# Kernel optimization log

Hardware: AMD Instinct MI355X
Metric: run time of the kernel (lower is better)

Reference implementation:

```python
import jax, jax.numpy as jnp
import numpy as np

N = 16384

def setup_inputs() -> dict:
    key = jax.random.key(0)
    k1, k2, k3 = jax.random.split(key, 3)
    risk_scores = jax.random.normal(k1, (N,), dtype=jnp.float32)
    survival_times = jax.random.normal(k2, (N,), dtype=jnp.float32)
    # 0/1 event indicator (1 = event observed, 0 = censored)
    events = (jax.random.uniform(k3, (N,)) < 0.5).astype(jnp.float32)
    return {"risk_scores": risk_scores, "survival_times": survival_times, "events": events}

def reference(risk_scores, survival_times, events):
    # Risk-set matrix: R[i, j] = 1 if T[j] >= T[i] (vectorized version of the
    # original O(n^2) double Python loop).
    R = (survival_times[None, :] >= survival_times[:, None]).astype(risk_scores.dtype)  # [n, n]
    exp_theta = jnp.exp(risk_scores)                # [n]
    # sum_j exp(theta_j) * R[i, j]  ->  matvec
    risk_set_sum = R @ exp_theta                    # [n]
    loss = -jnp.mean((risk_scores - jnp.log(risk_set_sum)) * events)
    return loss
```

## Files before the change

### kernel.cpp

```cpp
#include <hip/hip_runtime.h>
#include <math.h>

#define NF 16384
#define NB 4096
#define NBLK 64
#define TPB 256
#define CHUNK (NB/TPB)
#define NZ (4 + 3*NB)
#define BLOCK 256

__device__ __forceinline__ int bucket_of(float t) {
    int b = (int)((t + 6.0f) * (NB / 12.0f));
    return min(max(b, 0), NB - 1);
}

__global__ void surv_zero(int* __restrict__ w) {
    int i = blockIdx.x * TPB + threadIdx.x;
    if (i < NZ) w[i] = 0;
}

__global__ __launch_bounds__(TPB) void surv_pipe(
        const float* __restrict__ theta, const float* __restrict__ T,
        const float* __restrict__ events,
        int* __restrict__ bar, int* __restrict__ ticket, float* __restrict__ accum,
        int* __restrict__ hcnt, float* __restrict__ hE, int* __restrict__ rel,
        float2* __restrict__ sorted, float* __restrict__ out) {
    __shared__ int   pfx[NB + 1];
    __shared__ float sfx[NB];
    __shared__ int   sc[TPB];
    __shared__ float se[TPB];

    const int tid = threadIdx.x;
    const int i   = blockIdx.x * TPB + tid;

    const float Ti = T[i];
    const float Ei = expf(theta[i]);
    const int   bi = bucket_of(Ti);
    atomicAdd(&hcnt[bi], 1);
    atomicAdd(&hE[bi], Ei);

    __syncthreads();
    if (tid == 0) {
        __hip_atomic_fetch_add(&bar[0], 1, __ATOMIC_RELEASE, __HIP_MEMORY_SCOPE_AGENT);
        while (__hip_atomic_load(&bar[0], __ATOMIC_ACQUIRE, __HIP_MEMORY_SCOPE_AGENT) < NBLK)
            __builtin_amdgcn_s_sleep(8);
    }
    __syncthreads();

    int lc[CHUNK]; float le[CHUNK];
    const int base = tid * CHUNK;
    int cs = 0; float es = 0.f;
    #pragma unroll
    for (int k = 0; k < CHUNK; ++k) {
        lc[k] = hcnt[base + k];
        le[k] = hE[base + k];
        cs += lc[k]; es += le[k];
    }
    sc[tid] = cs; se[tid] = es;
    __syncthreads();
    for (int s = 1; s < TPB; s <<= 1) {
        int   a = (tid >= s)      ? sc[tid - s] : 0;
        float f = (tid + s < TPB) ? se[tid + s] : 0.f;
        __syncthreads();
        sc[tid] += a; se[tid] += f;
        __syncthreads();
    }
    {   int run = sc[tid] - cs;
        #pragma unroll
        for (int k = 0; k < CHUNK; ++k) { pfx[base + k] = run; run += lc[k]; }
        if (tid == TPB - 1) pfx[NB] = run;
    }
    {   float rs = se[tid] - es;
        #pragma unroll
        for (int k = CHUNK - 1; k >= 0; --k) { sfx[base + k] = rs; rs += le[k]; }
    }
    __syncthreads();

    const int pos = pfx[bi] + atomicAdd(&rel[bi], 1);
    sorted[pos] = make_float2(Ti, Ei);

    __syncthreads();
    if (tid == 0) {
        __hip_atomic_fetch_add(&bar[1], 1, __ATOMIC_RELEASE, __HIP_MEMORY_SCOPE_AGENT);
        while (__hip_atomic_load(&bar[1], __ATOMIC_ACQUIRE, __HIP_MEMORY_SCOPE_AGENT) < NBLK)
            __builtin_amdgcn_s_sleep(8);
    }
    __syncthreads();

    float risk = sfx[bi];
    const int p1 = pfx[bi + 1];
    for (int p = pfx[bi]; p < p1; ++p) {
        float2 v = sorted[p];
        risk += (v.x >= Ti) ? v.y : 0.f;
    }
    float term = (theta[i] - logf(risk)) * events[i];

    #pragma unroll
    for (int off = 32; off > 0; off >>= 1) term += __shfl_down(term, off, 64);
    if ((tid & 63) == 0) se[tid >> 6] = term;
    __syncthreads();
    if (tid == 0) {
        atomicAdd(accum, se[0] + se[1] + se[2] + se[3]);
        __threadfence();
        int t = atomicAdd(ticket, 1);
        if (t == NBLK - 1) {
            float tot = atomicAdd(accum, 0.f);
            out[0] = -tot / (float)NF;
        }
    }
}

__global__ void surv_partial_bf(const float* __restrict__ theta, const float* __restrict__ T,
                                const float* __restrict__ events, float* __restrict__ bsum, int n) {
    __shared__ float red[BLOCK];
    const int tid = threadIdx.x;
    const int i = blockIdx.x * BLOCK + tid;
    float term = 0.f;
    if (i < n) {
        const float Ti = T[i];
        float risk = 0.f;
        for (int j = 0; j < n; ++j)
            risk += (T[j] >= Ti) ? expf(theta[j]) : 0.f;
        term = (theta[i] - logf(risk)) * events[i];
    }
    red[tid] = term;
    __syncthreads();
    for (int s = BLOCK / 2; s > 0; s >>= 1) {
        if (tid < s) red[tid] += red[tid + s];
        __syncthreads();
    }
    if (tid == 0) bsum[blockIdx.x] = red[0];
}

__global__ void surv_final(const float* __restrict__ bsum, float* __restrict__ out,
                           int nblocks, int n) {
    float v = 0.f;
    for (int b = threadIdx.x; b < nblocks; b += 64) v += bsum[b];
    for (int off = 32; off > 0; off >>= 1) v += __shfl_down(v, off, 64);
    if (threadIdx.x == 0) out[0] = -v / (float)n;
}

extern "C" void kernel_launch(void* const* d_in, const int* in_sizes, int n_in,
                              void* d_out, int out_size, void* d_ws, size_t ws_size,
                              hipStream_t stream) {
    const float* theta  = (const float*)d_in[0];
    const float* T      = (const float*)d_in[1];
    const float* events = (const float*)d_in[2];
    float* out = (float*)d_out;
    const int n = in_sizes[0];

    const size_t need = ((size_t)2 * NF + NZ) * 4;
    const bool fast = (n == NF) && ((size_t)ws_size >= need);

    if (!fast) {
        const int nbi = (n + BLOCK - 1) / BLOCK;
        float* bsum = (float*)d_ws;
        surv_partial_bf<<<nbi, BLOCK, 0, stream>>>(theta, T, events, bsum, n);
        surv_final<<<1, 64, 0, stream>>>(bsum, out, nbi, n);
        return;
    }

    float2* sorted = (float2*)d_ws;
    int*    meta   = (int*)d_ws + 2 * NF;
    int*    bar    = meta;
    int*    ticket = meta + 2;
    float*  accum  = (float*)(meta + 3);
    int*    hcnt   = meta + 4;
    float*  hE     = (float*)(meta + 4 + NB);
    int*    rel    = meta + 4 + 2 * NB;

    const int zb = (NZ + TPB - 1) / TPB;
    surv_zero<<<zb, TPB, 0, stream>>>(meta);
    surv_pipe<<<NBLK, TPB, 0, stream>>>(theta, T, events, bar, ticket, accum,
                                        hcnt, hE, rel, sorted, out);
}
```

Measured before the change: 83.51 us.

## Split persistent grid-barrier kernel into three launches with memset init

Replaces the single persistent kernel, which used two software grid barriers built on spinning global atomics, with three separate kernels: histogram, scan+scatter, and risk/reduction. Kernel boundaries now provide the ordering, removing the spin-wait latency and its memory-fence costs. The zero kernel becomes a hipMemsetAsync. The final reduction now goes through per-block partial sums plus a last-block ticket instead of a single atomic accumulator. The trade-off is extra launch overhead, plus every block redoing the full 4096-bucket scan while only block 0 writes it to global memory.

Result: no change. 83.32 us (-0.2%).

```diff
diff --git a/kernel.cpp b/kernel.cpp
--- a/kernel.cpp
+++ b/kernel.cpp
@@ -3,10 +3,10 @@
 
 #define NF 16384
 #define NB 4096
-#define NBLK 64
 #define TPB 256
+#define NBLK (NF/TPB)
 #define CHUNK (NB/TPB)
-#define NZ (4 + 3*NB)
+#define NMETA (3*NB+1)
 #define BLOCK 256
 
 __device__ __forceinline__ int bucket_of(float t) {
@@ -14,45 +14,36 @@
     return min(max(b, 0), NB - 1);
 }
 
-__global__ void surv_zero(int* __restrict__ w) {
-    int i = blockIdx.x * TPB + threadIdx.x;
-    if (i < NZ) w[i] = 0;
+__global__ __launch_bounds__(TPB) void surv_hist(
+        const float* __restrict__ theta, const float* __restrict__ T,
+        float* __restrict__ Earr, int* __restrict__ cnt, float* __restrict__ hE) {
+    const int i = blockIdx.x * TPB + threadIdx.x;
+    const float Tv = T[i];
+    const float Ev = expf(theta[i]);
+    Earr[i] = Ev;
+    const int b = bucket_of(Tv);
+    atomicAdd(&cnt[b], 1);
+    atomicAdd(&hE[b], Ev);
 }
 
-__global__ __launch_bounds__(TPB) void surv_pipe(
-        const float* __restrict__ theta, const float* __restrict__ T,
-        const float* __restrict__ events,
-        int* __restrict__ bar, int* __restrict__ ticket, float* __restrict__ accum,
-        int* __restrict__ hcnt, float* __restrict__ hE, int* __restrict__ rel,
-        float2* __restrict__ sorted, float* __restrict__ out) {
+__global__ __launch_bounds__(TPB) void surv_scan_scatter(
+        const float* __restrict__ T, const float* __restrict__ Earr,
+        const int* __restrict__ cnt, const float* __restrict__ hE,
+        int* __restrict__ rel, int* __restrict__ pfxg, float* __restrict__ sfxg,
+        float2* __restrict__ sorted) {
     __shared__ int   pfx[NB + 1];
     __shared__ float sfx[NB];
     __shared__ int   sc[TPB];
     __shared__ float se[TPB];
 
-    const int tid = threadIdx.x;
-    const int i   = blockIdx.x * TPB + tid;
-
-    const float Ti = T[i];
-    const float Ei = expf(theta[i]);
-    const int   bi = bucket_of(Ti);
-    atomicAdd(&hcnt[bi], 1);
-    atomicAdd(&hE[bi], Ei);
-
-    __syncthreads();
-    if (tid == 0) {
-        __hip_atomic_fetch_add(&bar[0], 1, __ATOMIC_RELEASE, __HIP_MEMORY_SCOPE_AGENT);
-        while (__hip_atomic_load(&bar[0], __ATOMIC_ACQUIRE, __HIP_MEMORY_SCOPE_AGENT) < NBLK)
-            __builtin_amdgcn_s_sleep(8);
-    }
-    __syncthreads();
+    const int tid  = threadIdx.x;
+    const int base = tid * CHUNK;
 
     int lc[CHUNK]; float le[CHUNK];
-    const int base = tid * CHUNK;
     int cs = 0; float es = 0.f;
     #pragma unroll
     for (int k = 0; k < CHUNK; ++k) {
-        lc[k] = hcnt[base + k];
+        lc[k] = cnt[base + k];
         le[k] = hE[base + k];
         cs += lc[k]; es += le[k];
     }
@@ -76,37 +67,56 @@
     }
     __syncthreads();
 
-    const int pos = pfx[bi] + atomicAdd(&rel[bi], 1);
-    sorted[pos] = make_float2(Ti, Ei);
+    if (blockIdx.x == 0) {
+        for (int idx = tid; idx < NB + 1; idx += TPB) pfxg[idx] = pfx[idx];
+        for (int idx = tid; idx < NB;     idx += TPB) sfxg[idx] = sfx[idx];
+    }
 
-    __syncthreads();
-    if (tid == 0) {
-        __hip_atomic_fetch_add(&bar[1], 1, __ATOMIC_RELEASE, __HIP_MEMORY_SCOPE_AGENT);
-        while (__hip_atomic_load(&bar[1], __ATOMIC_ACQUIRE, __HIP_MEMORY_SCOPE_AGENT) < NBLK)
-            __builtin_amdgcn_s_sleep(8);
+    const int i = blockIdx.x * TPB + tid;
+    const float Tv = T[i];
+    const float Ev = Earr[i];
+    const int b = bucket_of(Tv);
+    const int pos = pfx[b] + atomicAdd(&rel[b], 1);
+    sorted[pos] = make_float2(Tv, Ev);
+}
+
+__global__ __launch_bounds__(TPB) void surv_risk(
+        const float* __restrict__ theta, const float* __restrict__ T,
+        const float* __restrict__ events,
+        const int* __restrict__ pfxg, const float* __restrict__ sfxg,
+        const float2* __restrict__ sorted,
+        float* __restrict__ bsum, int* __restrict__ ticket,
+        float* __restrict__ out) {
+    __shared__ float ws4[TPB / 64];
+    __shared__ int last;
+
+    const int tid = threadIdx.x;
+    const int i = blockIdx.x * TPB + tid;
+    const float Tv = T[i];
+    const int b = bucket_of(Tv);
+    float r = sfxg[b];
+    const int p1 = pfxg[b + 1];
+    for (int p = pfxg[b]; p < p1; ++p) {
+        float2 v = sorted[p];
+        r += (v.x >= Tv) ? v.y : 0.f;
     }
-    __syncthreads();
-
-    float risk = sfx[bi];
-    const int p1 = pfx[bi + 1];
-    for (int p = pfx[bi]; p < p1; ++p) {
-        float2 v = sorted[p];
-        risk += (v.x >= Ti) ? v.y : 0.f;
-    }
-    float term = (theta[i] - logf(risk)) * events[i];
+    float term = (theta[i] - logf(r)) * events[i];
 
     #pragma unroll
     for (int off = 32; off > 0; off >>= 1) term += __shfl_down(term, off, 64);
-    if ((tid & 63) == 0) se[tid >> 6] = term;
+    if ((tid & 63) == 0) ws4[tid >> 6] = term;
     __syncthreads();
     if (tid == 0) {
-        atomicAdd(accum, se[0] + se[1] + se[2] + se[3]);
+        bsum[blockIdx.x] = ws4[0] + ws4[1] + ws4[2] + ws4[3];
         __threadfence();
-        int t = atomicAdd(ticket, 1);
-        if (t == NBLK - 1) {
-            float tot = atomicAdd(accum, 0.f);
-            out[0] = -tot / (float)NF;
-        }
+        last = (atomicAdd(ticket, 1) == NBLK - 1) ? 1 : 0;
+    }
+    __syncthreads();
+    if (last && tid < 64) {
+        float v = atomicAdd(&bsum[tid], 0.f);
+        #pragma unroll
+        for (int off = 32; off > 0; off >>= 1) v += __shfl_down(v, off, 64);
+        if (tid == 0) out[0] = -v / (float)NF;
     }
 }
 
@@ -149,7 +159,7 @@
     float* out = (float*)d_out;
     const int n = in_sizes[0];
 
-    const size_t need = ((size_t)2 * NF + NZ) * 4;
+    const size_t need = ((size_t)3 * NF + (NB + 1) + NB + NBLK + NMETA) * 4;
     const bool fast = (n == NF) && ((size_t)ws_size >= need);
 
     if (!fast) {
@@ -161,16 +171,20 @@
     }
 
     float2* sorted = (float2*)d_ws;
-    int*    meta   = (int*)d_ws + 2 * NF;
-    int*    bar    = meta;
-    int*    ticket = meta + 2;
-    float*  accum  = (float*)(meta + 3);
-    int*    hcnt   = meta + 4;
-    float*  hE     = (float*)(meta + 4 + NB);
-    int*    rel    = meta + 4 + 2 * NB;
+    float*  Earr   = (float*)d_ws + 2 * NF;
+    int*    pfxg   = (int*)(Earr + NF);
+    float*  sfxg   = (float*)(pfxg + NB + 1);
+    float*  bsum   = sfxg + NB;
+    int*    meta   = (int*)(bsum + NBLK);
+    int*    cnt    = meta;
+    float*  hE     = (float*)(meta + NB);
+    int*    rel    = meta + 2 * NB;
+    int*    ticket = meta + 3 * NB;
 
-    const int zb = (NZ + TPB - 1) / TPB;
-    surv_zero<<<zb, TPB, 0, stream>>>(meta);
-    surv_pipe<<<NBLK, TPB, 0, stream>>>(theta, T, events, bar, ticket, accum,
-                                        hcnt, hE, rel, sorted, out);
+    hipMemsetAsync(meta, 0, (size_t)NMETA * 4, stream);
+    surv_hist<<<NBLK, TPB, 0, stream>>>(theta, T, Earr, cnt, hE);
+    surv_scan_scatter<<<NBLK, TPB, 0, stream>>>(T, Earr, cnt, hE, rel,
+                                                pfxg, sfxg, sorted);
+    surv_risk<<<NBLK, TPB, 0, stream>>>(theta, T, events, pfxg, sfxg, sorted,
+                                        bsum, ticket, out);
 }
```
